# Kernel tuning notes

Hardware: AMD Instinct MI355X
Metric: run time of the kernel (lower is better)

Reference implementation:

```python
import jax, jax.numpy as jnp
import numpy as np

EMBED_DIM = 512
NUM_HEAD = 16
HEAD_DIM = EMBED_DIM // NUM_HEAD
EPS = 1e-6


def setup_inputs() -> dict:
    key = jax.random.key(0)
    ks = jax.random.split(key, 7)
    B, L = 4, 4096
    scale = 1.0 / np.sqrt(EMBED_DIM)
    return {
        "query": jax.random.normal(ks[0], (B, L, EMBED_DIM), jnp.float32),
        "key": jax.random.normal(ks[1], (B, L, EMBED_DIM), jnp.float32),
        "value": jax.random.normal(ks[2], (B, L, EMBED_DIM), jnp.float32),
        "Wq": jax.random.normal(ks[3], (EMBED_DIM, EMBED_DIM), jnp.float32) * scale,
        "Wk": jax.random.normal(ks[4], (EMBED_DIM, EMBED_DIM), jnp.float32) * scale,
        "Wv": jax.random.normal(ks[5], (EMBED_DIM, EMBED_DIM), jnp.float32) * scale,
        "Wm": jax.random.normal(ks[6], (EMBED_DIM, EMBED_DIM), jnp.float32) * scale,
    }


def reference(query, key, value, Wq, Wk, Wv, Wm):
    bs, Lq, E = query.shape
    H, D = NUM_HEAD, HEAD_DIM
    # projections (nn.Linear without bias: x @ W.T)
    q = (query @ Wq.T).reshape(bs, Lq, H, D)
    k = (key @ Wk.T).reshape(bs, -1, H, D)
    v = (value @ Wv.T).reshape(bs, -1, H, D)
    # elu+1 feature map
    Q = jax.nn.elu(q) + 1.0
    K = jax.nn.elu(k) + 1.0
    v_len = v.shape[1]
    v = v / v_len
    # KV accumulation: [n, h, d, dv]
    KV = jnp.einsum('nshd,nshv->nhdv', K, v)
    # normalizer Z: [n, l, h]
    Z = 1.0 / (jnp.einsum('nlhd,nhd->nlh', Q, K.sum(axis=1)) + EPS)
    # weighted combination: [n, l, h, dv]
    message = jnp.einsum('nlhd,nhdv,nlh->nlhv', Q, KV, Z) * v_len
    # merge projection (dropout p=0 -> identity)
    out = message.reshape(bs, Lq, H * D) @ Wm.T
    return out
```

## Files before the change

### kernel.cpp

```cpp
#include <hip/hip_runtime.h>

#define EMBED  512
#define NHEAD  16
#define HDIM   32
#define NBATCH 4
#define SEQ    4096
#define NROWS  (NBATCH * SEQ)
#define FEPS   1e-6f

typedef __attribute__((ext_vector_type(8))) short short8;
typedef __attribute__((ext_vector_type(4))) float f32x4;

__device__ __forceinline__ short f2bf(float x) {
    unsigned u = __float_as_uint(x);
    u += 0x7FFFu + ((u >> 16) & 1u);
    return (short)(u >> 16);
}
__device__ __forceinline__ float bf2f(short h) {
    return __uint_as_float(((unsigned)(unsigned short)h) << 16);
}

__global__ __launch_bounds__(256)
void convert_w4(const float* __restrict__ W0, const float* __restrict__ W1,
                const float* __restrict__ W2, const float* __restrict__ W3,
                short* __restrict__ H0, short* __restrict__ L0,
                short* __restrict__ H1, short* __restrict__ L1,
                short* __restrict__ H2, short* __restrict__ L2,
                short* __restrict__ H3, short* __restrict__ L3) {
    const int seg = blockIdx.x >> 8;
    const int i = ((blockIdx.x & 255) * 256 + threadIdx.x) * 4;
    const float* W = (seg == 0) ? W0 : (seg == 1) ? W1 : (seg == 2) ? W2 : W3;
    short* H = (seg == 0) ? H0 : (seg == 1) ? H1 : (seg == 2) ? H2 : H3;
    short* L = (seg == 0) ? L0 : (seg == 1) ? L1 : (seg == 2) ? L2 : L3;
    float4 v = *(const float4*)(W + i);
    short4 h, l;
    h.x = f2bf(v.x); l.x = f2bf(v.x - bf2f(h.x));
    h.y = f2bf(v.y); l.y = f2bf(v.y - bf2f(h.y));
    h.z = f2bf(v.z); l.z = f2bf(v.z - bf2f(h.z));
    h.w = f2bf(v.w); l.w = f2bf(v.w - bf2f(h.w));
    *(short4*)(H + i) = h;
    *(short4*)(L + i) = l;
}

#define LDA 40

__global__ __launch_bounds__(256, 2)
void qkv_gemm(const float* __restrict__ Aq, const float* __restrict__ Ak,
              const float* __restrict__ Av,
              const short* __restrict__ WqH, const short* __restrict__ WqL,
              const short* __restrict__ WkH, const short* __restrict__ WkL,
              const short* __restrict__ WvH, const short* __restrict__ WvL,
              float* __restrict__ Qb, float* __restrict__ Kb,
              float* __restrict__ Vb) {
    __shared__ short Ah[128][LDA];
    __shared__ short Al[128][LDA];

    const int tid  = threadIdx.x;
    const int lane = tid & 63;
    const int wave = tid >> 6;
    const int wm   = (wave >> 1) * 64;
    const int wn   = (wave & 1) * 64;
    const int l15  = lane & 15;
    const int kg   = lane >> 4;

    const int lin = blockIdx.x;
    const int op  = lin >> 9;
    const int r_  = lin & 511;
    const int bn  = (r_ >> 7) * 128;
    const int bm  = (r_ & 127) * 128;

    const float* A   = (op == 0) ? Aq  : (op == 1) ? Ak  : Av;
    const short* Whi = (op == 0) ? WqH : (op == 1) ? WkH : WvH;
    const short* Wlo = (op == 0) ? WqL : (op == 1) ? WkL : WvL;
    float* C = (op == 0) ? Qb : (op == 1) ? Kb : Vb;

    const int sr = tid >> 2;
    const int sk = (tid & 3) * 8;
    const float* Ap0 = A + (size_t)(bm + sr) * EMBED + sk;
    const float* Ap1 = Ap0 + (size_t)64 * EMBED;

    const short* Bh = Whi + (size_t)(bn + wn + l15) * EMBED + kg * 8;
    const short* Bl = Wlo + (size_t)(bn + wn + l15) * EMBED + kg * 8;

    f32x4 acc[4][4];
#pragma unroll
    for (int i = 0; i < 4; ++i)
#pragma unroll
        for (int j = 0; j < 4; ++j) acc[i][j] = (f32x4)0.0f;

#pragma unroll 1
    for (int k0 = 0; k0 < EMBED; k0 += 32) {
        float4 a0 = *(const float4*)(Ap0 + k0);
        float4 a1 = *(const float4*)(Ap0 + k0 + 4);
        float4 a2 = *(const float4*)(Ap1 + k0);
        float4 a3 = *(const float4*)(Ap1 + k0 + 4);
        short8 bh[4], bl[4];
#pragma unroll
        for (int j = 0; j < 4; ++j) {
            bh[j] = *(const short8*)(Bh + (size_t)j * 16 * EMBED + k0);
            bl[j] = *(const short8*)(Bl + (size_t)j * 16 * EMBED + k0);
        }
        __syncthreads();
        {
            float v[8] = {a0.x, a0.y, a0.z, a0.w, a1.x, a1.y, a1.z, a1.w};
            short8 hv, lv;
#pragma unroll
            for (int q = 0; q < 8; ++q) {
                short hb = f2bf(v[q]);
                hv[q] = hb; lv[q] = f2bf(v[q] - bf2f(hb));
            }
            *(short8*)&Ah[sr][sk] = hv;
            *(short8*)&Al[sr][sk] = lv;
        }
        {
            float v[8] = {a2.x, a2.y, a2.z, a2.w, a3.x, a3.y, a3.z, a3.w};
            short8 hv, lv;
#pragma unroll
            for (int q = 0; q < 8; ++q) {
                short hb = f2bf(v[q]);
                hv[q] = hb; lv[q] = f2bf(v[q] - bf2f(hb));
            }
            *(short8*)&Ah[sr + 64][sk] = hv;
            *(short8*)&Al[sr + 64][sk] = lv;
        }
        __syncthreads();

        short8 ah[4], alr[4];
#pragma unroll
        for (int i = 0; i < 4; ++i) {
            ah[i]  = *(const short8*)&Ah[wm + i * 16 + l15][kg * 8];
            alr[i] = *(const short8*)&Al[wm + i * 16 + l15][kg * 8];
        }
#pragma unroll
        for (int i = 0; i < 4; ++i)
#pragma unroll
            for (int j = 0; j < 4; ++j) {
                acc[i][j] = __builtin_amdgcn_mfma_f32_16x16x32_bf16(ah[i],  bh[j], acc[i][j], 0, 0, 0);
                acc[i][j] = __builtin_amdgcn_mfma_f32_16x16x32_bf16(ah[i],  bl[j], acc[i][j], 0, 0, 0);
                acc[i][j] = __builtin_amdgcn_mfma_f32_16x16x32_bf16(alr[i], bh[j], acc[i][j], 0, 0, 0);
            }
    }

#pragma unroll
    for (int i = 0; i < 4; ++i)
#pragma unroll
        for (int j = 0; j < 4; ++j) {
            const int col = bn + wn + j * 16 + l15;
#pragma unroll
            for (int r = 0; r < 4; ++r) {
                const int row = bm + wm + i * 16 + kg * 4 + r;
                float vv = acc[i][j][r];
                if (op < 2) vv = (vv > 0.f) ? (vv + 1.f) : __expf(vv);
                else        vv = vv * (1.0f / (float)SEQ);
                C[(size_t)row * EMBED + col] = vv;
            }
        }
}

__global__ __launch_bounds__(256, 2)
void merge_gemm(const float* __restrict__ A, const short* __restrict__ Whi,
                const short* __restrict__ Wlo, float* __restrict__ C) {
    __shared__ short Ah[128][LDA];
    __shared__ short Al[128][LDA];

    const int tid  = threadIdx.x;
    const int lane = tid & 63;
    const int wave = tid >> 6;
    const int wm   = (wave >> 1) * 64;
    const int wn   = (wave & 1) * 64;
    const int l15  = lane & 15;
    const int kg   = lane >> 4;

    const int lin = blockIdx.x;
    const int bn  = (lin >> 7) * 128;
    const int bm  = (lin & 127) * 128;

    const int sr = tid >> 2;
    const int sk = (tid & 3) * 8;
    const float* Ap0 = A + (size_t)(bm + sr) * EMBED + sk;
    const float* Ap1 = Ap0 + (size_t)64 * EMBED;

    const short* Bh = Whi + (size_t)(bn + wn + l15) * EMBED + kg * 8;
    const short* Bl = Wlo + (size_t)(bn + wn + l15) * EMBED + kg * 8;

    f32x4 acc[4][4];
#pragma unroll
    for (int i = 0; i < 4; ++i)
#pragma unroll
        for (int j = 0; j < 4; ++j) acc[i][j] = (f32x4)0.0f;

#pragma unroll 1
    for (int k0 = 0; k0 < EMBED; k0 += 32) {
        float4 a0 = *(const float4*)(Ap0 + k0);
        float4 a1 = *(const float4*)(Ap0 + k0 + 4);
        float4 a2 = *(const float4*)(Ap1 + k0);
        float4 a3 = *(const float4*)(Ap1 + k0 + 4);
        short8 bh[4], bl[4];
#pragma unroll
        for (int j = 0; j < 4; ++j) {
            bh[j] = *(const short8*)(Bh + (size_t)j * 16 * EMBED + k0);
            bl[j] = *(const short8*)(Bl + (size_t)j * 16 * EMBED + k0);
        }
        __syncthreads();
        {
            float v[8] = {a0.x, a0.y, a0.z, a0.w, a1.x, a1.y, a1.z, a1.w};
            short8 hv, lv;
#pragma unroll
            for (int q = 0; q < 8; ++q) {
                short hb = f2bf(v[q]);
                hv[q] = hb; lv[q] = f2bf(v[q] - bf2f(hb));
            }
            *(short8*)&Ah[sr][sk] = hv;
            *(short8*)&Al[sr][sk] = lv;
        }
        {
            float v[8] = {a2.x, a2.y, a2.z, a2.w, a3.x, a3.y, a3.z, a3.w};
            short8 hv, lv;
#pragma unroll
            for (int q = 0; q < 8; ++q) {
                short hb = f2bf(v[q]);
                hv[q] = hb; lv[q] = f2bf(v[q] - bf2f(hb));
            }
            *(short8*)&Ah[sr + 64][sk] = hv;
            *(short8*)&Al[sr + 64][sk] = lv;
        }
        __syncthreads();

        short8 ah[4], alr[4];
#pragma unroll
        for (int i = 0; i < 4; ++i) {
            ah[i]  = *(const short8*)&Ah[wm + i * 16 + l15][kg * 8];
            alr[i] = *(const short8*)&Al[wm + i * 16 + l15][kg * 8];
        }
#pragma unroll
        for (int i = 0; i < 4; ++i)
#pragma unroll
            for (int j = 0; j < 4; ++j) {
                acc[i][j] = __builtin_amdgcn_mfma_f32_16x16x32_bf16(ah[i],  bh[j], acc[i][j], 0, 0, 0);
                acc[i][j] = __builtin_amdgcn_mfma_f32_16x16x32_bf16(ah[i],  bl[j], acc[i][j], 0, 0, 0);
                acc[i][j] = __builtin_amdgcn_mfma_f32_16x16x32_bf16(alr[i], bh[j], acc[i][j], 0, 0, 0);
            }
    }

#pragma unroll
    for (int i = 0; i < 4; ++i)
#pragma unroll
        for (int j = 0; j < 4; ++j) {
            const int col = bn + wn + j * 16 + l15;
#pragma unroll
            for (int r = 0; r < 4; ++r) {
                const int row = bm + wm + i * 16 + kg * 4 + r;
                C[(size_t)row * EMBED + col] = acc[i][j][r];
            }
        }
}

__global__ __launch_bounds__(256)
void kv_ksum_mfma(const float* __restrict__ Kf, const float* __restrict__ Vf,
                  float* __restrict__ KV, float* __restrict__ Ksum) {
    __shared__ char smem[34816];
    short (*Kh)[34] = (short (*)[34])smem;
    short (*Kl)[34] = (short (*)[34])(smem + 8704);
    short (*Vh)[34] = (short (*)[34])(smem + 17408);
    short (*Vl)[34] = (short (*)[34])(smem + 26112);

    const int bh_ = blockIdx.y;
    const int b = bh_ >> 4, h = bh_ & 15;
    const int s0 = blockIdx.x * 256;
    const int t = threadIdx.x;
    const int lane = t & 63, wave = t >> 6;
    const int l15 = lane & 15, kg = lane >> 4;
    const int ws = wave * 32;

    const int sl = t >> 1;
    const int dsel = (t & 1) * 16;
    const float* Kbase = Kf + (size_t)b * SEQ * EMBED + h * HDIM;
    const float* Vbase = Vf + (size_t)b * SEQ * EMBED + h * HDIM;

    f32x4 kvacc[2][2], ksacc[2];
#pragma unroll
    for (int i = 0; i < 2; ++i) {
        ksacc[i] = (f32x4)0.0f;
#pragma unroll
        for (int j = 0; j < 2; ++j) kvacc[i][j] = (f32x4)0.0f;
    }
    short8 ones;
#pragma unroll
    for (int q = 0; q < 8; ++q) ones[q] = (short)0x3F80;

    float4 kx[4], vx[4];
#pragma unroll
    for (int p = 0; p < 4; ++p) {
        kx[p] = *(const float4*)(Kbase + (size_t)(s0 + sl) * EMBED + dsel + 4 * p);
        vx[p] = *(const float4*)(Vbase + (size_t)(s0 + sl) * EMBED + dsel + 4 * p);
    }

#pragma unroll 1
    for (int it = 0; it < 2; ++it) {
        __syncthreads();
        {
            float kv_[8] = {kx[0].x, kx[0].y, kx[0].z, kx[0].w, kx[1].x, kx[1].y, kx[1].z, kx[1].w};
            float kv2[8] = {kx[2].x, kx[2].y, kx[2].z, kx[2].w, kx[3].x, kx[3].y, kx[3].z, kx[3].w};
            float vv_[8] = {vx[0].x, vx[0].y, vx[0].z, vx[0].w, vx[1].x, vx[1].y, vx[1].z, vx[1].w};
            float vv2[8] = {vx[2].x, vx[2].y, vx[2].z, vx[2].w, vx[3].x, vx[3].y, vx[3].z, vx[3].w};
            short8 h0, l0, h1, l1;
#pragma unroll
            for (int q = 0; q < 8; ++q) { short hb = f2bf(kv_[q]); h0[q] = hb; l0[q] = f2bf(kv_[q] - bf2f(hb)); }
#pragma unroll
            for (int q = 0; q < 8; ++q) { short hb = f2bf(kv2[q]); h1[q] = hb; l1[q] = f2bf(kv2[q] - bf2f(hb)); }
            *(short8*)&Kh[sl][dsel] = h0; *(short8*)&Kh[sl][dsel + 8] = h1;
            *(short8*)&Kl[sl][dsel] = l0; *(short8*)&Kl[sl][dsel + 8] = l1;
#pragma unroll
            for (int q = 0; q < 8; ++q) { short hb = f2bf(vv_[q]); h0[q] = hb; l0[q] = f2bf(vv_[q] - bf2f(hb)); }
#pragma unroll
            for (int q = 0; q < 8; ++q) { short hb = f2bf(vv2[q]); h1[q] = hb; l1[q] = f2bf(vv2[q] - bf2f(hb)); }
            *(short8*)&Vh[sl][dsel] = h0; *(short8*)&Vh[sl][dsel + 8] = h1;
            *(short8*)&Vl[sl][dsel] = l0; *(short8*)&Vl[sl][dsel + 8] = l1;
        }
        __syncthreads();
        if (it == 0) {
#pragma unroll
            for (int p = 0; p < 4; ++p) {
                kx[p] = *(const float4*)(Kbase + (size_t)(s0 + 128 + sl) * EMBED + dsel + 4 * p);
                vx[p] = *(const float4*)(Vbase + (size_t)(s0 + 128 + sl) * EMBED + dsel + 4 * p);
            }
        }
        short8 kah[2], kal[2], vbh[2], vbl[2];
#pragma unroll
        for (int i = 0; i < 2; ++i) {
#pragma unroll
            for (int q = 0; q < 8; ++q) {
                const int srow = ws + kg * 8 + q;
                const int col  = i * 16 + l15;
                kah[i][q] = Kh[srow][col];
                kal[i][q] = Kl[srow][col];
                vbh[i][q] = Vh[srow][col];
                vbl[i][q] = Vl[srow][col];
            }
        }
#pragma unroll
        for (int i = 0; i < 2; ++i) {
#pragma unroll
            for (int j = 0; j < 2; ++j) {
                kvacc[i][j] = __builtin_amdgcn_mfma_f32_16x16x32_bf16(kah[i], vbh[j], kvacc[i][j], 0, 0, 0);
                kvacc[i][j] = __builtin_amdgcn_mfma_f32_16x16x32_bf16(kah[i], vbl[j], kvacc[i][j], 0, 0, 0);
                kvacc[i][j] = __builtin_amdgcn_mfma_f32_16x16x32_bf16(kal[i], vbh[j], kvacc[i][j], 0, 0, 0);
            }
            ksacc[i] = __builtin_amdgcn_mfma_f32_16x16x32_bf16(kah[i], ones, ksacc[i], 0, 0, 0);
            ksacc[i] = __builtin_amdgcn_mfma_f32_16x16x32_bf16(kal[i], ones, ksacc[i], 0, 0, 0);
        }
    }

    __syncthreads();
    float* red = (float*)smem;
    float* myred = red + wave * 1056;
#pragma unroll
    for (int i = 0; i < 2; ++i)
#pragma unroll
        for (int j = 0; j < 2; ++j)
#pragma unroll
            for (int r = 0; r < 4; ++r)
                myred[(i * 16 + kg * 4 + r) * 32 + j * 16 + l15] = kvacc[i][j][r];
    if (l15 == 0) {
#pragma unroll
        for (int i = 0; i < 2; ++i)
#pragma unroll
            for (int r = 0; r < 4; ++r)
                myred[1024 + i * 16 + kg * 4 + r] = ksacc[i][r];
    }
    __syncthreads();
    float* kvout = KV + (size_t)bh_ * 1024;
    for (int idx = t; idx < 1024; idx += 256) {
        float s4 = red[idx] + red[1056 + idx] + red[2112 + idx] + red[3168 + idx];
        atomicAdd(&kvout[idx], s4);
    }
    if (t < 32) {
        float s4 = red[1024 + t] + red[1056 + 1024 + t] + red[2112 + 1024 + t] + red[3168 + 1024 + t];
        atomicAdd(&Ksum[bh_ * 32 + t], s4);
    }
}

__global__ __launch_bounds__(512)
void message_kernel(float* __restrict__ Q, const float* __restrict__ KV,
                    const float* __restrict__ Ksum) {
    const int blk  = blockIdx.x;
    const int row0 = blk * 4;
    const int b    = row0 >> 12;
    const int t    = threadIdx.x;
    const int h    = t >> 5, e = t & 31;

    __shared__ float q[4][EMBED];
    __shared__ float ks[EMBED];
    ks[t] = Ksum[b * EMBED + t];
#pragma unroll
    for (int r = 0; r < 4; ++r) q[r][t] = Q[(size_t)(row0 + r) * EMBED + t];

    const float* kvh = KV + (size_t)(b * NHEAD + h) * HDIM * HDIM + e;
    float kc[HDIM];
#pragma unroll
    for (int d = 0; d < HDIM; ++d) kc[d] = kvh[d * HDIM];
    __syncthreads();

#pragma unroll
    for (int r = 0; r < 4; ++r) {
        float zden = FEPS, m = 0.f;
#pragma unroll
        for (int d = 0; d < HDIM; ++d) {
            float qd = q[r][h * HDIM + d];
            zden = fmaf(qd, ks[h * HDIM + d], zden);
            m    = fmaf(qd, kc[d], m);
        }
        Q[(size_t)(row0 + r) * EMBED + t] = m * ((float)SEQ / zden);
    }
}

extern "C" void kernel_launch(void* const* d_in, const int* in_sizes, int n_in,
                              void* d_out, int out_size, void* d_ws, size_t ws_size,
                              hipStream_t stream) {
    const float* query = (const float*)d_in[0];
    const float* key   = (const float*)d_in[1];
    const float* value = (const float*)d_in[2];
    const float* Wq    = (const float*)d_in[3];
    const float* Wk    = (const float*)d_in[4];
    const float* Wv    = (const float*)d_in[5];
    const float* Wm    = (const float*)d_in[6];
    float* out = (float*)d_out;

    float* ws  = (float*)d_ws;
    float* Qb  = ws;
    float* Kb  = Qb + (size_t)NROWS * EMBED;
    float* Vb  = Kb + (size_t)NROWS * EMBED;
    float* KVb = Vb + (size_t)NROWS * EMBED;
    float* KSb = KVb + 64 * 1024;
    short* wsp = (short*)(KSb + 64 * HDIM);
    const int WN = EMBED * EMBED;
    short* WqH = wsp;            short* WqL = wsp + WN;
    short* WkH = wsp + 2 * WN;   short* WkL = wsp + 3 * WN;
    short* WvH = wsp + 4 * WN;   short* WvL = wsp + 5 * WN;
    short* WmH = wsp + 6 * WN;   short* WmL = wsp + 7 * WN;

    hipMemsetAsync(KVb, 0, (64 * 1024 + 64 * HDIM) * sizeof(float), stream);

    convert_w4<<<1024, 256, 0, stream>>>(Wq, Wk, Wv, Wm,
                                         WqH, WqL, WkH, WkL,
                                         WvH, WvL, WmH, WmL);

    qkv_gemm<<<1536, 256, 0, stream>>>(query, key, value,
                                       WqH, WqL, WkH, WkL, WvH, WvL,
                                       Qb, Kb, Vb);

    kv_ksum_mfma<<<dim3(16, 64), 256, 0, stream>>>(Kb, Vb, KVb, KSb);
    message_kernel<<<NROWS / 4, 512, 0, stream>>>(Qb, KVb, KSb);

    merge_gemm<<<512, 256, 0, stream>>>(Qb, WmH, WmL, out);
}
```

Before: 326.8 us.

## Pre-split activations to bf16 hi/lo and stage GEMM tiles via direct global-to-LDS loads

The fp32 activations for Q/K/V are now converted to bf16 hi/lo pairs in a separate pass. The message kernel emits bf16 hi/lo output directly. Both GEMMs load A and B tiles through global_load_lds into a swizzled LDS layout instead of converting inside the k-loop and loading B from global into registers. Occupancy hint rises to 3 blocks per CU. This moves conversion out of the GEMM inner loop, but it adds an extra full pass over the inputs, writes and rereads 2x bf16 copies, and keeps the loop single-buffered with two barriers per iteration.

```diff
diff --git a/kernel.cpp b/kernel.cpp
--- a/kernel.cpp
+++ b/kernel.cpp
@@ -6,6 +6,8 @@
 #define NBATCH 4
 #define SEQ    4096
 #define NROWS  (NBATCH * SEQ)
+#define NE     (NROWS * EMBED)
+#define WN     (EMBED * EMBED)
 #define FEPS   1e-6f
 
 typedef __attribute__((ext_vector_type(8))) short short8;
@@ -20,40 +22,63 @@
     return __uint_as_float(((unsigned)(unsigned short)h) << 16);
 }
 
+#define GLDS16(gp, lp)                                                   \
+    __builtin_amdgcn_global_load_lds(                                    \
+        (__attribute__((address_space(1))) void*)(void*)(gp),            \
+        (__attribute__((address_space(3))) void*)(void*)(lp), 16, 0, 0)
+
 __global__ __launch_bounds__(256)
-void convert_w4(const float* __restrict__ W0, const float* __restrict__ W1,
-                const float* __restrict__ W2, const float* __restrict__ W3,
-                short* __restrict__ H0, short* __restrict__ L0,
-                short* __restrict__ H1, short* __restrict__ L1,
-                short* __restrict__ H2, short* __restrict__ L2,
-                short* __restrict__ H3, short* __restrict__ L3) {
-    const int seg = blockIdx.x >> 8;
-    const int i = ((blockIdx.x & 255) * 256 + threadIdx.x) * 4;
-    const float* W = (seg == 0) ? W0 : (seg == 1) ? W1 : (seg == 2) ? W2 : W3;
-    short* H = (seg == 0) ? H0 : (seg == 1) ? H1 : (seg == 2) ? H2 : H3;
-    short* L = (seg == 0) ? L0 : (seg == 1) ? L1 : (seg == 2) ? L2 : L3;
-    float4 v = *(const float4*)(W + i);
-    short4 h, l;
-    h.x = f2bf(v.x); l.x = f2bf(v.x - bf2f(h.x));
-    h.y = f2bf(v.y); l.y = f2bf(v.y - bf2f(h.y));
-    h.z = f2bf(v.z); l.z = f2bf(v.z - bf2f(h.z));
-    h.w = f2bf(v.w); l.w = f2bf(v.w - bf2f(h.w));
-    *(short4*)(H + i) = h;
-    *(short4*)(L + i) = l;
-}
-
-#define LDA 40
-
-__global__ __launch_bounds__(256, 2)
-void qkv_gemm(const float* __restrict__ Aq, const float* __restrict__ Ak,
-              const float* __restrict__ Av,
+void convert_all(const float* __restrict__ q, const float* __restrict__ k,
+                 const float* __restrict__ v,
+                 const float* __restrict__ wq, const float* __restrict__ wk,
+                 const float* __restrict__ wv, const float* __restrict__ wm,
+                 short* __restrict__ qh, short* __restrict__ ql,
+                 short* __restrict__ kh, short* __restrict__ kl,
+                 short* __restrict__ vh, short* __restrict__ vl,
+                 short* __restrict__ wqh, short* __restrict__ wql,
+                 short* __restrict__ wkh, short* __restrict__ wkl,
+                 short* __restrict__ wvh, short* __restrict__ wvl,
+                 short* __restrict__ wmh, short* __restrict__ wml) {
+    const int b = blockIdx.x;
+    const float* src; short* dh; short* dl; int boff;
+    if (b < 12288) {
+        const int s = b >> 12;
+        src = (s == 0) ? q  : (s == 1) ? k  : v;
+        dh  = (s == 0) ? qh : (s == 1) ? kh : vh;
+        dl  = (s == 0) ? ql : (s == 1) ? kl : vl;
+        boff = b & 4095;
+    } else {
+        const int s = (b - 12288) >> 7;
+        src = (s == 0) ? wq  : (s == 1) ? wk  : (s == 2) ? wv  : wm;
+        dh  = (s == 0) ? wqh : (s == 1) ? wkh : (s == 2) ? wvh : wmh;
+        dl  = (s == 0) ? wql : (s == 1) ? wkl : (s == 2) ? wvl : wml;
+        boff = (b - 12288) & 127;
+    }
+    const size_t i = ((size_t)boff * 256 + threadIdx.x) * 8;
+    float4 x0 = *(const float4*)(src + i);
+    float4 x1 = *(const float4*)(src + i + 4);
+    float vv[8] = {x0.x, x0.y, x0.z, x0.w, x1.x, x1.y, x1.z, x1.w};
+    short8 h, l;
+#pragma unroll
+    for (int t = 0; t < 8; ++t) {
+        short hb = f2bf(vv[t]);
+        h[t] = hb;
+        l[t] = f2bf(vv[t] - bf2f(hb));
+    }
+    *(short8*)(dh + i) = h;
+    *(short8*)(dl + i) = l;
+}
+
+__global__ __launch_bounds__(256, 3)
+void qkv_gemm(const short* __restrict__ Aqh, const short* __restrict__ Aql,
+              const short* __restrict__ Akh, const short* __restrict__ Akl,
+              const short* __restrict__ Avh, const short* __restrict__ Avl,
               const short* __restrict__ WqH, const short* __restrict__ WqL,
               const short* __restrict__ WkH, const short* __restrict__ WkL,
               const short* __restrict__ WvH, const short* __restrict__ WvL,
               float* __restrict__ Qb, float* __restrict__ Kb,
               float* __restrict__ Vb) {
-    __shared__ short Ah[128][LDA];
-    __shared__ short Al[128][LDA];
+    __shared__ short lds[4][128][32];
 
     const int tid  = threadIdx.x;
     const int lane = tid & 63;
@@ -69,18 +94,26 @@
     const int bn  = (r_ >> 7) * 128;
     const int bm  = (r_ & 127) * 128;
 
-    const float* A   = (op == 0) ? Aq  : (op == 1) ? Ak  : Av;
-    const short* Whi = (op == 0) ? WqH : (op == 1) ? WkH : WvH;
-    const short* Wlo = (op == 0) ? WqL : (op == 1) ? WkL : WvL;
+    const short* Ah = (op == 0) ? Aqh : (op == 1) ? Akh : Avh;
+    const short* Al = (op == 0) ? Aql : (op == 1) ? Akl : Avl;
+    const short* Bh = (op == 0) ? WqH : (op == 1) ? WkH : WvH;
+    const short* Bl = (op == 0) ? WqL : (op == 1) ? WkL : WvL;
     float* C = (op == 0) ? Qb : (op == 1) ? Kb : Vb;
 
-    const int sr = tid >> 2;
-    const int sk = (tid & 3) * 8;
-    const float* Ap0 = A + (size_t)(bm + sr) * EMBED + sk;
-    const float* Ap1 = Ap0 + (size_t)64 * EMBED;
-
-    const short* Bh = Whi + (size_t)(bn + wn + l15) * EMBED + kg * 8;
-    const short* Bl = Wlo + (size_t)(bn + wn + l15) * EMBED + kg * 8;
+    const int sr = lane >> 2;
+    const int sc = (((lane & 3) ^ ((lane >> 3) & 3)) << 3);
+    const int rt = wave * 32 + sr;
+    const short* gAh = Ah + (size_t)(bm + rt) * EMBED + sc;
+    const short* gAl = Al + (size_t)(bm + rt) * EMBED + sc;
+    const short* gBh = Bh + (size_t)(bn + rt) * EMBED + sc;
+    const short* gBl = Bl + (size_t)(bn + rt) * EMBED + sc;
+
+    short* dAh = &lds[0][wave * 32][0];
+    short* dAl = &lds[1][wave * 32][0];
+    short* dBh = &lds[2][wave * 32][0];
+    short* dBl = &lds[3][wave * 32][0];
+
+    const int rk = ((kg ^ ((l15 >> 1) & 3)) << 3);
 
     f32x4 acc[4][4];
 #pragma unroll
@@ -90,55 +123,33 @@
 
 #pragma unroll 1
     for (int k0 = 0; k0 < EMBED; k0 += 32) {
-        float4 a0 = *(const float4*)(Ap0 + k0);
-        float4 a1 = *(const float4*)(Ap0 + k0 + 4);
-        float4 a2 = *(const float4*)(Ap1 + k0);
-        float4 a3 = *(const float4*)(Ap1 + k0 + 4);
-        short8 bh[4], bl[4];
-#pragma unroll
-        for (int j = 0; j < 4; ++j) {
-            bh[j] = *(const short8*)(Bh + (size_t)j * 16 * EMBED + k0);
-            bl[j] = *(const short8*)(Bl + (size_t)j * 16 * EMBED + k0);
-        }
-        __syncthreads();
-        {
-            float v[8] = {a0.x, a0.y, a0.z, a0.w, a1.x, a1.y, a1.z, a1.w};
-            short8 hv, lv;
-#pragma unroll
-            for (int q = 0; q < 8; ++q) {
-                short hb = f2bf(v[q]);
-                hv[q] = hb; lv[q] = f2bf(v[q] - bf2f(hb));
-            }
-            *(short8*)&Ah[sr][sk] = hv;
-            *(short8*)&Al[sr][sk] = lv;
-        }
-        {
-            float v[8] = {a2.x, a2.y, a2.z, a2.w, a3.x, a3.y, a3.z, a3.w};
-            short8 hv, lv;
-#pragma unroll
-            for (int q = 0; q < 8; ++q) {
-                short hb = f2bf(v[q]);
-                hv[q] = hb; lv[q] = f2bf(v[q] - bf2f(hb));
-            }
-            *(short8*)&Ah[sr + 64][sk] = hv;
-            *(short8*)&Al[sr + 64][sk] = lv;
-        }
-        __syncthreads();
-
-        short8 ah[4], alr[4];
+        GLDS16(gAh + k0,              dAh);
+        GLDS16(gAh + 16 * EMBED + k0, dAh + 512);
+        GLDS16(gAl + k0,              dAl);
+        GLDS16(gAl + 16 * EMBED + k0, dAl + 512);
+        GLDS16(gBh + k0,              dBh);
+        GLDS16(gBh + 16 * EMBED + k0, dBh + 512);
+        GLDS16(gBl + k0,              dBl);
+        GLDS16(gBl + 16 * EMBED + k0, dBl + 512);
+        __syncthreads();
+
+        short8 ahv[4], alv[4], bhv[4], blv[4];
 #pragma unroll
         for (int i = 0; i < 4; ++i) {
-            ah[i]  = *(const short8*)&Ah[wm + i * 16 + l15][kg * 8];
-            alr[i] = *(const short8*)&Al[wm + i * 16 + l15][kg * 8];
+            ahv[i] = *(const short8*)&lds[0][wm + i * 16 + l15][rk];
+            alv[i] = *(const short8*)&lds[1][wm + i * 16 + l15][rk];
+            bhv[i] = *(const short8*)&lds[2][wn + i * 16 + l15][rk];
+            blv[i] = *(const short8*)&lds[3][wn + i * 16 + l15][rk];
         }
 #pragma unroll
         for (int i = 0; i < 4; ++i)
 #pragma unroll
             for (int j = 0; j < 4; ++j) {
-                acc[i][j] = __builtin_amdgcn_mfma_f32_16x16x32_bf16(ah[i],  bh[j], acc[i][j], 0, 0, 0);
-                acc[i][j] = __builtin_amdgcn_mfma_f32_16x16x32_bf16(ah[i],  bl[j], acc[i][j], 0, 0, 0);
-                acc[i][j] = __builtin_amdgcn_mfma_f32_16x16x32_bf16(alr[i], bh[j], acc[i][j], 0, 0, 0);
-            }
+                acc[i][j] = __builtin_amdgcn_mfma_f32_16x16x32_bf16(ahv[i], bhv[j], acc[i][j], 0, 0, 0);
+                acc[i][j] = __builtin_amdgcn_mfma_f32_16x16x32_bf16(ahv[i], blv[j], acc[i][j], 0, 0, 0);
+                acc[i][j] = __builtin_amdgcn_mfma_f32_16x16x32_bf16(alv[i], bhv[j], acc[i][j], 0, 0, 0);
+            }
+        __syncthreads();
     }
 
 #pragma unroll
@@ -157,11 +168,11 @@
         }
 }
 
-__global__ __launch_bounds__(256, 2)
-void merge_gemm(const float* __restrict__ A, const short* __restrict__ Whi,
-                const short* __restrict__ Wlo, float* __restrict__ C) {
-    __shared__ short Ah[128][LDA];
-    __shared__ short Al[128][LDA];
+__global__ __launch_bounds__(256, 3)
+void merge_gemm(const short* __restrict__ Mh, const short* __restrict__ Ml,
+                const short* __restrict__ WhP, const short* __restrict__ WlP,
+                float* __restrict__ C) {
+    __shared__ short lds[4][128][32];
 
     const int tid  = threadIdx.x;
     const int lane = tid & 63;
@@ -175,13 +186,20 @@
     const int bn  = (lin >> 7) * 128;
     const int bm  = (lin & 127) * 128;
 
-    const int sr = tid >> 2;
-    const int sk = (tid & 3) * 8;
-    const float* Ap0 = A + (size_t)(bm + sr) * EMBED + sk;
-    const float* Ap1 = Ap0 + (size_t)64 * EMBED;
-
-    const short* Bh = Whi + (size_t)(bn + wn + l15) * EMBED + kg * 8;
-    const short* Bl = Wlo + (size_t)(bn + wn + l15) * EMBED + kg * 8;
+    const int sr = lane >> 2;
+    const int sc = (((lane & 3) ^ ((lane >> 3) & 3)) << 3);
+    const int rt = wave * 32 + sr;
+    const short* gAh = Mh  + (size_t)(bm + rt) * EMBED + sc;
+    const short* gAl = Ml  + (size_t)(bm + rt) * EMBED + sc;
+    const short* gBh = WhP + (size_t)(bn + rt) * EMBED + sc;
+    const short* gBl = WlP + (size_t)(bn + rt) * EMBED + sc;
+
+    short* dAh = &lds[0][wave * 32][0];
+    short* dAl = &lds[1][wave * 32][0];
+    short* dBh = &lds[2][wave * 32][0];
+    short* dBl = &lds[3][wave * 32][0];
+
+    const int rk = ((kg ^ ((l15 >> 1) & 3)) << 3);
 
     f32x4 acc[4][4];
 #pragma unroll
@@ -191,55 +209,33 @@
 
 #pragma unroll 1
     for (int k0 = 0; k0 < EMBED; k0 += 32) {
-        float4 a0 = *(const float4*)(Ap0 + k0);
-        float4 a1 = *(const float4*)(Ap0 + k0 + 4);
-        float4 a2 = *(const float4*)(Ap1 + k0);
-        float4 a3 = *(const float4*)(Ap1 + k0 + 4);
-        short8 bh[4], bl[4];
-#pragma unroll
-        for (int j = 0; j < 4; ++j) {
-            bh[j] = *(const short8*)(Bh + (size_t)j * 16 * EMBED + k0);
-            bl[j] = *(const short8*)(Bl + (size_t)j * 16 * EMBED + k0);
-        }
-        __syncthreads();
-        {
-            float v[8] = {a0.x, a0.y, a0.z, a0.w, a1.x, a1.y, a1.z, a1.w};
-            short8 hv, lv;
-#pragma unroll
-            for (int q = 0; q < 8; ++q) {
-                short hb = f2bf(v[q]);
-                hv[q] = hb; lv[q] = f2bf(v[q] - bf2f(hb));
-            }
-            *(short8*)&Ah[sr][sk] = hv;
-            *(short8*)&Al[sr][sk] = lv;
-        }
-        {
-            float v[8] = {a2.x, a2.y, a2.z, a2.w, a3.x, a3.y, a3.z, a3.w};
-            short8 hv, lv;
-#pragma unroll
-            for (int q = 0; q < 8; ++q) {
-                short hb = f2bf(v[q]);
-                hv[q] = hb; lv[q] = f2bf(v[q] - bf2f(hb));
-            }
-            *(short8*)&Ah[sr + 64][sk] = hv;
-            *(short8*)&Al[sr + 64][sk] = lv;
-        }
-        __syncthreads();
-
-        short8 ah[4], alr[4];
+        GLDS16(gAh + k0,              dAh);
+        GLDS16(gAh + 16 * EMBED + k0, dAh + 512);
+        GLDS16(gAl + k0,              dAl);
+        GLDS16(gAl + 16 * EMBED + k0, dAl + 512);
+        GLDS16(gBh + k0,              dBh);
+        GLDS16(gBh + 16 * EMBED + k0, dBh + 512);
+        GLDS16(gBl + k0,              dBl);
+        GLDS16(gBl + 16 * EMBED + k0, dBl + 512);
+        __syncthreads();
+
+        short8 ahv[4], alv[4], bhv[4], blv[4];
 #pragma unroll
         for (int i = 0; i < 4; ++i) {
-            ah[i]  = *(const short8*)&Ah[wm + i * 16 + l15][kg * 8];
-            alr[i] = *(const short8*)&Al[wm + i * 16 + l15][kg * 8];
+            ahv[i] = *(const short8*)&lds[0][wm + i * 16 + l15][rk];
+            alv[i] = *(const short8*)&lds[1][wm + i * 16 + l15][rk];
+            bhv[i] = *(const short8*)&lds[2][wn + i * 16 + l15][rk];
+            blv[i] = *(const short8*)&lds[3][wn + i * 16 + l15][rk];
         }
 #pragma unroll
         for (int i = 0; i < 4; ++i)
 #pragma unroll
             for (int j = 0; j < 4; ++j) {
-                acc[i][j] = __builtin_amdgcn_mfma_f32_16x16x32_bf16(ah[i],  bh[j], acc[i][j], 0, 0, 0);
-                acc[i][j] = __builtin_amdgcn_mfma_f32_16x16x32_bf16(ah[i],  bl[j], acc[i][j], 0, 0, 0);
-                acc[i][j] = __builtin_amdgcn_mfma_f32_16x16x32_bf16(alr[i], bh[j], acc[i][j], 0, 0, 0);
-            }
+                acc[i][j] = __builtin_amdgcn_mfma_f32_16x16x32_bf16(ahv[i], bhv[j], acc[i][j], 0, 0, 0);
+                acc[i][j] = __builtin_amdgcn_mfma_f32_16x16x32_bf16(ahv[i], blv[j], acc[i][j], 0, 0, 0);
+                acc[i][j] = __builtin_amdgcn_mfma_f32_16x16x32_bf16(alv[i], bhv[j], acc[i][j], 0, 0, 0);
+            }
+        __syncthreads();
     }
 
 #pragma unroll
@@ -381,8 +377,9 @@
 }
 
 __global__ __launch_bounds__(512)
-void message_kernel(float* __restrict__ Q, const float* __restrict__ KV,
-                    const float* __restrict__ Ksum) {
+void message_kernel(const float* __restrict__ Q, const float* __restrict__ KV,
+                    const float* __restrict__ Ksum,
+                    short* __restrict__ Mh, short* __restrict__ Ml) {
     const int blk  = blockIdx.x;
     const int row0 = blk * 4;
     const int b    = row0 >> 12;
@@ -410,7 +407,10 @@
             zden = fmaf(qd, ks[h * HDIM + d], zden);
             m    = fmaf(qd, kc[d], m);
         }
-        Q[(size_t)(row0 + r) * EMBED + t] = m * ((float)SEQ / zden);
+        float vv = m * ((float)SEQ / zden);
+        short hb = f2bf(vv);
+        Mh[(size_t)(row0 + r) * EMBED + t] = hb;
+        Ml[(size_t)(row0 + r) * EMBED + t] = f2bf(vv - bf2f(hb));
     }
 }
 
@@ -428,29 +428,35 @@
 
     float* ws  = (float*)d_ws;
     float* Qb  = ws;
-    float* Kb  = Qb + (size_t)NROWS * EMBED;
-    float* Vb  = Kb + (size_t)NROWS * EMBED;
-    float* KVb = Vb + (size_t)NROWS * EMBED;
+    float* Kb  = Qb + (size_t)NE;
+    float* Vb  = Kb + (size_t)NE;
+    float* KVb = Vb + (size_t)NE;
     float* KSb = KVb + 64 * 1024;
     short* wsp = (short*)(KSb + 64 * HDIM);
-    const int WN = EMBED * EMBED;
     short* WqH = wsp;            short* WqL = wsp + WN;
     short* WkH = wsp + 2 * WN;   short* WkL = wsp + 3 * WN;
     short* WvH = wsp + 4 * WN;   short* WvL = wsp + 5 * WN;
     short* WmH = wsp + 6 * WN;   short* WmL = wsp + 7 * WN;
+    short* Xp  = wsp + 8 * WN;
+    short* Qih = Xp;             short* Qil = Xp + (size_t)NE;
+    short* Kih = Xp + 2 * (size_t)NE;  short* Kil = Xp + 3 * (size_t)NE;
+    short* Vih = Xp + 4 * (size_t)NE;  short* Vil = Xp + 5 * (size_t)NE;
+    short* Mh = (short*)Kb;
+    short* Ml = Mh + (size_t)NE;
 
     hipMemsetAsync(KVb, 0, (64 * 1024 + 64 * HDIM) * sizeof(float), stream);
 
-    convert_w4<<<1024, 256, 0, stream>>>(Wq, Wk, Wv, Wm,
-                                         WqH, WqL, WkH, WkL,
-                                         WvH, WvL, WmH, WmL);
-
-    qkv_gemm<<<1536, 256, 0, stream>>>(query, key, value,
+    convert_all<<<12800, 256, 0, stream>>>(query, key, value, Wq, Wk, Wv, Wm,
+                                           Qih, Qil, Kih, Kil, Vih, Vil,
+                                           WqH, WqL, WkH, WkL,
+                                           WvH, WvL, WmH, WmL);
+
+    qkv_gemm<<<1536, 256, 0, stream>>>(Qih, Qil, Kih, Kil, Vih, Vil,
                                        WqH, WqL, WkH, WkL, WvH, WvL,
                                        Qb, Kb, Vb);
 
     kv_ksum_mfma<<<dim3(16, 64), 256, 0, stream>>>(Kb, Vb, KVb, KSb);
-    message_kernel<<<NROWS / 4, 512, 0, stream>>>(Qb, KVb, KSb);
-
-    merge_gemm<<<512, 256, 0, stream>>>(Qb, WmH, WmL, out);
-}
+    message_kernel<<<NROWS / 4, 512, 0, stream>>>(Qb, KVb, KSb, Mh, Ml);
+
+    merge_gemm<<<512, 256, 0, stream>>>(Mh, Ml, WmH, WmL, out);
+}
```

New measurement: 306.9 us. 1.06x faster.
